# Kernel tuning notes

Measured on AMD Instinct MI355X. Metric: run time of the kernel, lower is better.

## Reference

```python
import jax, jax.numpy as jnp
import numpy as np

H, W, C = 192, 192, 1024

def setup_inputs() -> dict:
    key = jax.random.key(0)
    k1, k2 = jax.random.split(key)
    x = jax.random.normal(k1, (1, H, W, C), dtype=jnp.float32)
    gamma = jax.random.normal(k2, (1,), dtype=jnp.float32)
    return {"x": x, "gamma": gamma}

def reference(x, gamma):
    b, h, w, c = x.shape
    # NOTE: faithful to the TF code: a pure reshape of NHWC into (1, C, H*W),
    # with NO transpose (the original relies on reshape semantics).
    proj = x.reshape(1, c, h * w)                      # query == key^T == value
    energy = jnp.einsum('bcn,bdn->bcd', proj, proj)    # (1, C, C)
    energy_new = jnp.max(energy, axis=-1, keepdims=True) - energy  # sign-flipped
    attention = jax.nn.softmax(energy_new, axis=-1)    # (1, C, C)
    out = jnp.einsum('bcd,bdn->bcn', attention, proj)  # (1, C, H*W)
    out = out.reshape(1, h, w, c)
    return gamma * out + x
```

## Files before the change

kernel.cpp:

```cpp
#include <hip/hip_runtime.h>
#include <cstdint>

#define C_DIM 1024
#define N_DIM 36864

typedef unsigned short ushort_t;
typedef __attribute__((ext_vector_type(8))) short bf16x8;
typedef __attribute__((ext_vector_type(4))) float f32x4;

__device__ __forceinline__ ushort_t f2b(float f) {
    unsigned u = __float_as_uint(f);
    u = (u + 0x7fffu + ((u >> 16) & 1u)) >> 16;
    return (ushort_t)u;
}
__device__ __forceinline__ float b2f(ushort_t b) {
    return __uint_as_float(((unsigned)b) << 16);
}

__device__ __forceinline__ void async16(const void* g, const void* lds) {
    __builtin_amdgcn_global_load_lds(
        (const __attribute__((address_space(1))) unsigned int*)(uintptr_t)g,
        (__attribute__((address_space(3))) unsigned int*)(uint32_t)(uintptr_t)lds,
        16, 0, 0);
}


__global__ __launch_bounds__(256) void k_convert(const float* __restrict__ x,
                                                 ushort_t* __restrict__ ph,
                                                 ushort_t* __restrict__ pl) {
    int i = blockIdx.x * 256 + threadIdx.x;
    float4 v = ((const float4*)x)[i];
    ushort4 h, l;
    h.x = f2b(v.x); l.x = f2b(v.x - b2f(h.x));
    h.y = f2b(v.y); l.y = f2b(v.y - b2f(h.y));
    h.z = f2b(v.z); l.z = f2b(v.z - b2f(h.z));
    h.w = f2b(v.w); l.w = f2b(v.w - b2f(h.w));
    ((ushort4*)ph)[i] = h;
    ((ushort4*)pl)[i] = l;
}

__global__ __launch_bounds__(256) void k_convtrans(const float* __restrict__ x,
                                                   ushort_t* __restrict__ ph,
                                                   ushort_t* __restrict__ pl,
                                                   ushort_t* __restrict__ pht) {
    __shared__ __align__(16) ushort_t th[64][72];
    const int t = threadIdx.x;
    const int i = t >> 2, qd = t & 3;
    const int c0 = blockIdx.y << 6;
    const size_t n0 = (size_t)blockIdx.x << 6;

    const size_t row = (size_t)(c0 + i) * N_DIM + n0 + (qd << 4);
    const float* src = x + row;
    union { ushort_t s[16]; uint4 q[2]; } H, Lo;
#pragma unroll
    for (int u4 = 0; u4 < 4; ++u4) {
        float4 v = ((const float4*)src)[u4];
        ushort_t h0 = f2b(v.x), h1 = f2b(v.y), h2 = f2b(v.z), h3 = f2b(v.w);
        H.s[u4 * 4 + 0] = h0; Lo.s[u4 * 4 + 0] = f2b(v.x - b2f(h0));
        H.s[u4 * 4 + 1] = h1; Lo.s[u4 * 4 + 1] = f2b(v.y - b2f(h1));
        H.s[u4 * 4 + 2] = h2; Lo.s[u4 * 4 + 2] = f2b(v.z - b2f(h2));
        H.s[u4 * 4 + 3] = h3; Lo.s[u4 * 4 + 3] = f2b(v.w - b2f(h3));
    }
    *(uint4*)(ph + row)     = H.q[0];
    *(uint4*)(ph + row + 8) = H.q[1];
    *(uint4*)(pl + row)     = Lo.q[0];
    *(uint4*)(pl + row + 8) = Lo.q[1];
    *(uint4*)&th[i][qd << 4]       = H.q[0];
    *(uint4*)&th[i][(qd << 4) + 8] = H.q[1];
    __syncthreads();

    ushort_t tmp[16];
#pragma unroll
    for (int u = 0; u < 16; ++u) tmp[u] = th[(qd << 4) + u][i];
    ushort_t* dst = pht + (n0 + i) * C_DIM + c0 + (qd << 4);
    *(uint4*)dst       = *(uint4*)tmp;
    *(uint4*)(dst + 8) = *(uint4*)(tmp + 8);
}

__global__ __launch_bounds__(256, 2) void k_egemm(const ushort_t* __restrict__ ph,
                                                  const ushort_t* __restrict__ pl,
                                                  float* __restrict__ g1,
                                                  float* __restrict__ g2,
                                                  int kchunk) {
    __shared__ __align__(16) ushort_t sAh[2][128 * 32];
    __shared__ __align__(16) ushort_t sAl[2][128 * 32];
    __shared__ __align__(16) ushort_t sBh[2][128 * 32];
    __shared__ __align__(16) ushort_t sBl[2][128 * 32];

    const int f   = blockIdx.x;
    const int xcd = f & 7;
    const int r   = f >> 3;
    const int z   = r / 5;
    const int s   = r - z * 5;
    const int chunk = (xcd + ((z & 1) << 2)) & 7;
    if (chunk >= 4 && s == 4) return;
    const int u = (chunk < 4) ? (chunk * 5 + s) : (20 + (chunk - 4) * 4 + s);

    int pr = u, pi = 0;
    while (pr >= 8 - pi) { pr -= 8 - pi; ++pi; }
    const int c0 = pi << 7;
    const int d0 = (pi + pr) << 7;

    const int t = threadIdx.x;
    const int w = t >> 6;
    const int L = t & 63;

    const int kb = z * kchunk;
    const int lrow = L >> 2;
    const int lcol = (((L & 3) ^ ((L >> 3) & 3)) << 3);

    const size_t rA = (size_t)(c0 + (w << 5) + lrow) * N_DIM + kb + lcol;
    const size_t rB = (size_t)(d0 + (w << 5) + lrow) * N_DIM + kb + lcol;
    const ushort_t* gAh = ph + rA;
    const ushort_t* gAl = pl + rA;
    const ushort_t* gBh = ph + rB;
    const ushort_t* gBl = pl + rB;
    const int wb = w << 10;

    const int wm = (w >> 1) << 6;
    const int wn = (w & 1) << 6;
    const int lm = L & 15, q = L >> 4;
    const int co = ((q ^ ((lm >> 1) & 3)) << 3);

    f32x4 acc1[4][4], acc2[4][4];
#pragma unroll
    for (int a = 0; a < 4; ++a)
#pragma unroll
        for (int b = 0; b < 4; ++b) { acc1[a][b] = (f32x4)0.0f; acc2[a][b] = (f32x4)0.0f; }

    auto stage = [&](int ti, int b) {
        const int o = ti << 5;
        async16(gAh + o,              sAh[b] + wb);
        async16(gAh + o + 16 * N_DIM, sAh[b] + wb + 512);
        async16(gAl + o,              sAl[b] + wb);
        async16(gAl + o + 16 * N_DIM, sAl[b] + wb + 512);
        async16(gBh + o,              sBh[b] + wb);
        async16(gBh + o + 16 * N_DIM, sBh[b] + wb + 512);
        async16(gBl + o,              sBl[b] + wb);
        async16(gBl + o + 16 * N_DIM, sBl[b] + wb + 512);
    };

    const int nIter = kchunk >> 5;
    stage(0, 0);

    for (int ti = 0; ti < nIter; ++ti) {
        const int cb = ti & 1;
        if (ti + 1 < nIter) {
            stage(ti + 1, cb ^ 1);
            __builtin_amdgcn_s_waitcnt(0x0F78);
        } else {
            __builtin_amdgcn_s_waitcnt(0x0F70);
        }
        __builtin_amdgcn_s_barrier();

        bf16x8 ah[4], al[4], bh[4], bl[4];
#pragma unroll
        for (int mt = 0; mt < 4; ++mt) {
            const int ro = ((wm + (mt << 4) + lm) << 5) + co;
            ah[mt] = *(const bf16x8*)(sAh[cb] + ro);
            al[mt] = *(const bf16x8*)(sAl[cb] + ro);
        }
#pragma unroll
        for (int nt = 0; nt < 4; ++nt) {
            const int ro = ((wn + (nt << 4) + lm) << 5) + co;
            bh[nt] = *(const bf16x8*)(sBh[cb] + ro);
            bl[nt] = *(const bf16x8*)(sBl[cb] + ro);
        }
#pragma unroll
        for (int mt = 0; mt < 4; ++mt)
#pragma unroll
            for (int nt = 0; nt < 4; ++nt) {
                acc1[mt][nt] = __builtin_amdgcn_mfma_f32_16x16x32_bf16(ah[mt], bh[nt], acc1[mt][nt], 0, 0, 0);
                acc2[mt][nt] = __builtin_amdgcn_mfma_f32_16x16x32_bf16(ah[mt], bl[nt], acc2[mt][nt], 0, 0, 0);
                acc2[mt][nt] = __builtin_amdgcn_mfma_f32_16x16x32_bf16(al[mt], bh[nt], acc2[mt][nt], 0, 0, 0);
            }
        __builtin_amdgcn_s_barrier();
    }

    const size_t base = ((size_t)z * 36 + u) << 14;
#pragma unroll
    for (int mt = 0; mt < 4; ++mt)
#pragma unroll
        for (int nt = 0; nt < 4; ++nt)
#pragma unroll
            for (int r2 = 0; r2 < 4; ++r2) {
                int lr = wm + (mt << 4) + (q << 2) + r2;
                int lc = wn + (nt << 4) + lm;
                size_t o = base + ((size_t)lr << 7) + lc;
                g1[o] = acc1[mt][nt][r2];
                g2[o] = acc2[mt][nt][r2];
            }
}

__global__ __launch_bounds__(256) void k_reduce(const float* __restrict__ g1,
                                                const float* __restrict__ g2,
                                                float* __restrict__ E,
                                                int splitk) {
    __shared__ float ld[64][65];
    const int t = threadIdx.x;
    const int i = t >> 2;
    const int jb = (t & 3) << 4;

    int pr = blockIdx.x, ci = 0;
    while (pr >= 16 - ci) { pr -= 16 - ci; ++ci; }
    const int cb = ci, db = ci + pr;
    const int i8 = cb >> 1, j8 = db >> 1;
    const int p = i8 * (17 - i8) / 2 + (j8 - i8);
    const size_t tbase = ((size_t)p << 14) + ((size_t)(cb & 1) << 13) + ((size_t)(db & 1) << 6);

    float acc[16];
#pragma unroll
    for (int u = 0; u < 16; ++u) acc[u] = 0.0f;

    for (int z = 0; z < splitk; ++z) {
        const size_t zo = (size_t)z * (36 << 14) + tbase + ((size_t)i << 7) + jb;
        const float* p1 = g1 + zo;
        const float* p2 = g2 + zo;
#pragma unroll
        for (int u4 = 0; u4 < 4; ++u4) {
            float4 v1 = ((const float4*)p1)[u4];
            float4 v2 = ((const float4*)p2)[u4];
            acc[u4 * 4 + 0] += v1.x + v2.x;
            acc[u4 * 4 + 1] += v1.y + v2.y;
            acc[u4 * 4 + 2] += v1.z + v2.z;
            acc[u4 * 4 + 3] += v1.w + v2.w;
        }
    }

    float* eo = E + ((size_t)((cb << 6) + i) << 10) + (db << 6) + jb;
#pragma unroll
    for (int u4 = 0; u4 < 4; ++u4) {
        float4 v;
        v.x = acc[u4 * 4 + 0]; v.y = acc[u4 * 4 + 1];
        v.z = acc[u4 * 4 + 2]; v.w = acc[u4 * 4 + 3];
        ((float4*)eo)[u4] = v;
    }

    if (cb != db) {
#pragma unroll
        for (int u4 = 0; u4 < 4; ++u4)
            *(float4*)&ld[i][jb + u4 * 4] = *(float4*)&acc[u4 * 4];
        __syncthreads();
        float tmp[16];
#pragma unroll
        for (int u = 0; u < 16; ++u) tmp[u] = ld[jb + u][i];
        float* et = E + ((size_t)((db << 6) + i) << 10) + (cb << 6) + jb;
#pragma unroll
        for (int u4 = 0; u4 < 4; ++u4)
            ((float4*)et)[u4] = *(float4*)&tmp[u4 * 4];
    }
}

__global__ __launch_bounds__(256) void k_softmax(const float* __restrict__ E,
                                                 ushort_t* __restrict__ att) {
    const int c = blockIdx.x;
    const int t = threadIdx.x;
    __shared__ float red[4];
    __shared__ float bcast;

    float4 e4 = ((const float4*)E)[((size_t)c << 8) + t];
    float m = fminf(fminf(e4.x, e4.y), fminf(e4.z, e4.w));
#pragma unroll
    for (int off = 32; off > 0; off >>= 1) m = fminf(m, __shfl_down(m, off));
    if ((t & 63) == 0) red[t >> 6] = m;
    __syncthreads();
    if (t == 0) bcast = fminf(fminf(red[0], red[1]), fminf(red[2], red[3]));
    __syncthreads();
    m = bcast;

    float w0 = expf(m - e4.x), w1 = expf(m - e4.y);
    float w2 = expf(m - e4.z), w3 = expf(m - e4.w);
    float s = w0 + w1 + w2 + w3;
#pragma unroll
    for (int off = 32; off > 0; off >>= 1) s += __shfl_down(s, off);
    if ((t & 63) == 0) red[t >> 6] = s;
    __syncthreads();
    if (t == 0) bcast = red[0] + red[1] + red[2] + red[3];
    __syncthreads();
    float inv = 1.0f / bcast;
    ushort4 o;
    o.x = f2b(w0 * inv); o.y = f2b(w1 * inv);
    o.z = f2b(w2 * inv); o.w = f2b(w3 * inv);
    ((ushort4*)att)[((size_t)c << 8) + t] = o;
}

__global__ __launch_bounds__(256) void k_transpose(const ushort_t* __restrict__ ph,
                                                   ushort_t* __restrict__ pht) {
    __shared__ __align__(16) ushort_t tile[64][72];
    const int t = threadIdx.x;
    const int i = t >> 2, qd = t & 3;
    const int c0 = blockIdx.y << 6;
    const size_t n0 = (size_t)blockIdx.x << 6;

    const ushort_t* src = ph + (size_t)(c0 + i) * N_DIM + n0 + (qd << 4);
    uint4 v0 = *(const uint4*)src;
    uint4 v1 = *(const uint4*)(src + 8);
    *(uint4*)&tile[i][qd << 4]       = v0;
    *(uint4*)&tile[i][(qd << 4) + 8] = v1;
    __syncthreads();

    ushort_t tmp[16];
#pragma unroll
    for (int u = 0; u < 16; ++u) tmp[u] = tile[(qd << 4) + u][i];
    ushort_t* dst = pht + (n0 + i) * C_DIM + c0 + (qd << 4);
    *(uint4*)dst       = *(uint4*)tmp;
    *(uint4*)(dst + 8) = *(uint4*)(tmp + 8);
}

__global__ __launch_bounds__(256, 2) void k_ogemm(const ushort_t* __restrict__ att,
                                                  const ushort_t* __restrict__ pht,
                                                  const float* __restrict__ x,
                                                  const float* __restrict__ gamma,
                                                  float* __restrict__ out) {
    __shared__ __align__(16) ushort_t sA[2][128 * 32];
    __shared__ __align__(16) ushort_t sB[2][256 * 32];

    const int d   = blockIdx.x;
    const int xcd = d & 7;
    const int r   = d >> 3;
    const int a0  = r >> 3;
    const int cbk = r & 7;
    const int n0 = (xcd * 18 + a0) << 8;
    const int c0 = cbk << 7;

    const int t = threadIdx.x;
    const int w = t >> 6, L = t & 63;
    const int srow = L >> 2;
    const int scol = (((L & 3) ^ ((L >> 3) & 3)) << 3);

    const int wm = (w >> 1) << 6;
    const int wn = (w & 1) << 7;
    const int lm = L & 15, q = L >> 4;
    const int co = ((q ^ ((lm >> 1) & 3)) << 3);

    f32x4 acc[4][8];
#pragma unroll
    for (int a = 0; a < 4; ++a)
#pragma unroll
        for (int b = 0; b < 8; ++b) acc[a][b] = (f32x4)0.0f;

    auto stage = [&](int k0, int b) {
#pragma unroll
        for (int j = 0; j < 6; ++j) {
            int ch = w * 6 + j;
            const ushort_t* src;
            ushort_t* base;
            if (ch < 8) {
                src = att + (size_t)(c0 + (ch << 4) + srow) * C_DIM + k0 + scol;
                base = sA[b] + (ch << 9);
            } else {
                int rb = ch - 8;
                src = pht + (size_t)(n0 + (rb << 4) + srow) * C_DIM + k0 + scol;
                base = sB[b] + (rb << 9);
            }
            async16(src, base);
        }
    };

    const int nIter = C_DIM / 32;
    stage(0, 0);

    for (int ti = 0; ti < nIter; ++ti) {
        const int cb = ti & 1;
        if (ti + 1 < nIter) {
            stage((ti + 1) << 5, cb ^ 1);
            __builtin_amdgcn_s_waitcnt(0x0F76);
        } else {
            __builtin_amdgcn_s_waitcnt(0x0F70);
        }
        __builtin_amdgcn_s_barrier();

        bf16x8 a[4], b[8];
#pragma unroll
        for (int mt = 0; mt < 4; ++mt)
            a[mt] = *(const bf16x8*)(sA[cb] + ((wm + (mt << 4) + lm) << 5) + co);
#pragma unroll
        for (int nt = 0; nt < 8; ++nt)
            b[nt] = *(const bf16x8*)(sB[cb] + ((wn + (nt << 4) + lm) << 5) + co);
#pragma unroll
        for (int mt = 0; mt < 4; ++mt)
#pragma unroll
            for (int nt = 0; nt < 8; ++nt)
                acc[mt][nt] = __builtin_amdgcn_mfma_f32_16x16x32_bf16(a[mt], b[nt], acc[mt][nt], 0, 0, 0);
        __builtin_amdgcn_s_barrier();
    }

    const float g = gamma[0];
#pragma unroll
    for (int mt = 0; mt < 4; ++mt)
#pragma unroll
        for (int nt = 0; nt < 8; ++nt)
#pragma unroll
            for (int r2 = 0; r2 < 4; ++r2) {
                int cg = c0 + wm + (mt << 4) + (q << 2) + r2;
                int ng = n0 + wn + (nt << 4) + lm;
                size_t o = (size_t)cg * N_DIM + ng;
                out[o] = g * acc[mt][nt][r2] + x[o];
            }
}

extern "C" void kernel_launch(void* const* d_in, const int* in_sizes, int n_in,
                              void* d_out, int out_size, void* d_ws, size_t ws_size,
                              hipStream_t stream) {
    const float* x     = (const float*)d_in[0];
    const float* gamma = (const float*)d_in[1];
    float* out = (float*)d_out;
    char* ws = (char*)d_ws;

    const size_t P  = 75497472ull;
    const size_t GT = 2359296ull;
    const size_t EB = 4194304ull, AT = 2097152ull;

    auto need = [&](int s, bool f) {
        return (size_t)(f ? 3 : 2) * P + (size_t)s * 2 * GT + EB + AT;
    };

    int S = 12;
    bool fused = true;
    if (ws_size < need(12, true)) {
        if      (ws_size >= need(8, true)) S = 8;
        else if (ws_size >= need(4, true)) S = 4;
        else {
            fused = false; S = 12;
            if (ws_size < need(12, false)) S = 8;
            if (ws_size < need(8,  false)) S = 4;
        }
    }
    const int kchunk = N_DIM / S;

    if (fused) {
        ushort_t* ph  = (ushort_t*)(ws);
        ushort_t* pl  = (ushort_t*)(ws + P);
        ushort_t* pht = (ushort_t*)(ws + 2 * P);
        float*    g1  = (float*)   (ws + 3 * P);
        float*    g2  = (float*)   (ws + 3 * P + (size_t)S * GT);
        float*    E   = (float*)   (ws + 3 * P + (size_t)S * 2 * GT);
        ushort_t* att = (ushort_t*)(ws + 3 * P + (size_t)S * 2 * GT + EB);

        k_convtrans<<<dim3(N_DIM / 64, C_DIM / 64), 256, 0, stream>>>(x, ph, pl, pht);
        k_egemm<<<dim3(40 * S), 256, 0, stream>>>(ph, pl, g1, g2, kchunk);
        k_reduce<<<dim3(136), 256, 0, stream>>>(g1, g2, E, S);
        k_softmax<<<dim3(C_DIM), 256, 0, stream>>>(E, att);
        k_ogemm<<<dim3(1152), 256, 0, stream>>>(att, pht, x, gamma, out);
    } else {
        ushort_t* ph  = (ushort_t*)(ws);
        ushort_t* pl  = (ushort_t*)(ws + P);
        float*    g1  = (float*)   (ws + 2 * P);
        float*    g2  = (float*)   (ws + 2 * P + (size_t)S * GT);
        float*    E   = (float*)   (ws + 2 * P + (size_t)S * 2 * GT);
        ushort_t* att = (ushort_t*)(ws + 2 * P + (size_t)S * 2 * GT + EB);
        ushort_t* pht = pl;

        k_convert<<<dim3((C_DIM * (size_t)N_DIM / 4) / 256), 256, 0, stream>>>(x, ph, pl);
        k_egemm<<<dim3(40 * S), 256, 0, stream>>>(ph, pl, g1, g2, kchunk);
        k_reduce<<<dim3(136), 256, 0, stream>>>(g1, g2, E, S);
        k_softmax<<<dim3(C_DIM), 256, 0, stream>>>(E, att);
        k_transpose<<<dim3(N_DIM / 64, C_DIM / 64), 256, 0, stream>>>(ph, pht);
        k_ogemm<<<dim3(1152), 256, 0, stream>>>(att, pht, x, gamma, out);
    }
}
```

Baseline: 585.0 us.

## Software-pipeline GEMM main loop with interleaved LDS reads, async stages and MFMA quadrants

Restructures the split-bf16 Gram GEMM inner loop into four phases that interleave LDS fragment reads, the async global-to-LDS prefetch of the next tile (split into A and B halves), and MFMA quadrants. The previous tile's last quadrant is deferred into the next iteration, and s_setprio raises wave priority around the MFMA blocks. The aim is to hide LDS and global latency behind matrix math instead of waiting on everything up front. In exchange it adds more barriers per iteration and fragile waitcnt and buffer-reuse ordering.

```diff
diff --git a/kernel.cpp b/kernel.cpp
--- a/kernel.cpp
+++ b/kernel.cpp
@@ -128,54 +128,87 @@
 #pragma unroll
         for (int b = 0; b < 4; ++b) { acc1[a][b] = (f32x4)0.0f; acc2[a][b] = (f32x4)0.0f; }
 
-    auto stage = [&](int ti, int b) {
+    auto stageA = [&](int ti, int b) {
         const int o = ti << 5;
         async16(gAh + o,              sAh[b] + wb);
         async16(gAh + o + 16 * N_DIM, sAh[b] + wb + 512);
         async16(gAl + o,              sAl[b] + wb);
         async16(gAl + o + 16 * N_DIM, sAl[b] + wb + 512);
+    };
+    auto stageB = [&](int ti, int b) {
+        const int o = ti << 5;
         async16(gBh + o,              sBh[b] + wb);
         async16(gBh + o + 16 * N_DIM, sBh[b] + wb + 512);
         async16(gBl + o,              sBl[b] + wb);
         async16(gBl + o + 16 * N_DIM, sBl[b] + wb + 512);
     };
 
+    bf16x8 ah[4], al[4], bh[4], bl[4];
+
+#define RD_A(i) { const int ro = ((wm + ((i) << 4) + lm) << 5) + co; \
+                  ah[i] = *(const bf16x8*)(pAh + ro); al[i] = *(const bf16x8*)(pAl + ro); }
+#define RD_B(i) { const int ro = ((wn + ((i) << 4) + lm) << 5) + co; \
+                  bh[i] = *(const bf16x8*)(pBh + ro); bl[i] = *(const bf16x8*)(pBl + ro); }
+#define CELL(m, n) { \
+    acc1[m][n] = __builtin_amdgcn_mfma_f32_16x16x32_bf16(ah[m], bh[n], acc1[m][n], 0, 0, 0); \
+    acc2[m][n] = __builtin_amdgcn_mfma_f32_16x16x32_bf16(ah[m], bl[n], acc2[m][n], 0, 0, 0); \
+    acc2[m][n] = __builtin_amdgcn_mfma_f32_16x16x32_bf16(al[m], bh[n], acc2[m][n], 0, 0, 0); }
+#define QUAD(m0, n0) { CELL(m0, n0) CELL(m0, (n0)+1) CELL((m0)+1, n0) CELL((m0)+1, (n0)+1) }
+#define LGKM0 __builtin_amdgcn_s_waitcnt(0xC07F)
+#define VM0   __builtin_amdgcn_s_waitcnt(0x0F70)
+#define BAR   __builtin_amdgcn_s_barrier()
+#define PRIO1 __builtin_amdgcn_s_setprio(1)
+#define PRIO0 __builtin_amdgcn_s_setprio(0)
+
     const int nIter = kchunk >> 5;
-    stage(0, 0);
+    stageA(0, 0); stageB(0, 0);
+    VM0;
+    BAR;
 
     for (int ti = 0; ti < nIter; ++ti) {
         const int cb = ti & 1;
-        if (ti + 1 < nIter) {
-            stage(ti + 1, cb ^ 1);
-            __builtin_amdgcn_s_waitcnt(0x0F78);
-        } else {
-            __builtin_amdgcn_s_waitcnt(0x0F70);
-        }
-        __builtin_amdgcn_s_barrier();
-
-        bf16x8 ah[4], al[4], bh[4], bl[4];
-#pragma unroll
-        for (int mt = 0; mt < 4; ++mt) {
-            const int ro = ((wm + (mt << 4) + lm) << 5) + co;
-            ah[mt] = *(const bf16x8*)(sAh[cb] + ro);
-            al[mt] = *(const bf16x8*)(sAl[cb] + ro);
-        }
-#pragma unroll
-        for (int nt = 0; nt < 4; ++nt) {
-            const int ro = ((wn + (nt << 4) + lm) << 5) + co;
-            bh[nt] = *(const bf16x8*)(sBh[cb] + ro);
-            bl[nt] = *(const bf16x8*)(sBl[cb] + ro);
-        }
-#pragma unroll
-        for (int mt = 0; mt < 4; ++mt)
-#pragma unroll
-            for (int nt = 0; nt < 4; ++nt) {
-                acc1[mt][nt] = __builtin_amdgcn_mfma_f32_16x16x32_bf16(ah[mt], bh[nt], acc1[mt][nt], 0, 0, 0);
-                acc2[mt][nt] = __builtin_amdgcn_mfma_f32_16x16x32_bf16(ah[mt], bl[nt], acc2[mt][nt], 0, 0, 0);
-                acc2[mt][nt] = __builtin_amdgcn_mfma_f32_16x16x32_bf16(al[mt], bh[nt], acc2[mt][nt], 0, 0, 0);
-            }
-        __builtin_amdgcn_s_barrier();
-    }
+        const ushort_t* pAh = sAh[cb];
+        const ushort_t* pAl = sAl[cb];
+        const ushort_t* pBh = sBh[cb];
+        const ushort_t* pBl = sBl[cb];
+        const bool pf = (ti + 1 < nIter);
+
+        RD_A(0) RD_A(1) RD_B(0) RD_B(1)
+        if (pf) stageA(ti + 1, cb ^ 1);
+        BAR;
+        LGKM0;
+        if (ti) { PRIO1; QUAD(2, 2) PRIO0; }
+        BAR;
+
+        RD_B(2) RD_B(3)
+        if (pf) stageB(ti + 1, cb ^ 1);
+        BAR;
+        LGKM0;
+        PRIO1; QUAD(0, 0) PRIO0;
+        BAR;
+
+        RD_A(2) RD_A(3)
+        BAR;
+        LGKM0;
+        PRIO1; QUAD(0, 2) PRIO0;
+        BAR;
+
+        if (pf) VM0;
+        BAR;
+        PRIO1; QUAD(2, 0) PRIO0;
+        BAR;
+    }
+    PRIO1; QUAD(2, 2) PRIO0;
+
+#undef RD_A
+#undef RD_B
+#undef CELL
+#undef QUAD
+#undef LGKM0
+#undef VM0
+#undef BAR
+#undef PRIO1
+#undef PRIO0
 
     const size_t base = ((size_t)z * 36 + u) << 14;
 #pragma unroll
```

Result: no change. 591.7 us (+1.2%).
